# Optimization experiments

Measured on AMD Instinct MI355X. Metric: run time of the kernel, lower is better.

Reference implementation:

```python
import jax, jax.numpy as jnp
import numpy as np

B, G = 128, 20000
HID = 64
NUM_BINS = 10
LEAKY_SLOPE = 0.01  # torch nn.LeakyReLU default


def setup_inputs() -> dict:
    key = jax.random.key(0)
    k1, k2, k3, k4, k5, k6 = jax.random.split(key, 6)
    vals = jax.random.normal(k1, (B, G), dtype=jnp.float32)
    keep = jax.random.uniform(k2, (B, G)) < 0.1
    expr_value = jnp.where(keep, vals, 0.0)
    # MLP params: Linear(1 -> HID), Linear(HID -> NUM_BINS-1)
    W1 = jax.random.normal(k3, (1, HID), dtype=jnp.float32) * 0.5
    b1 = jax.random.normal(k4, (HID,), dtype=jnp.float32) * 0.1
    W2 = jax.random.normal(k5, (HID, NUM_BINS - 1), dtype=jnp.float32) * (1.0 / np.sqrt(HID))
    b2 = jax.random.normal(k6, (NUM_BINS - 1,), dtype=jnp.float32) * 0.1
    return {"expr_value": expr_value, "W1": W1, "b1": b1, "W2": W2, "b2": b2}


def reference(expr_value, W1, b1, W2, b2):
    # mask of nonzero expression positions (B, G)
    mask_expr = (expr_value != 0).astype(jnp.float32)
    # tiny MLP applied to every position (vectorized; zero positions masked out below)
    x = expr_value[..., None]                      # (B, G, 1)
    h = x * W1[0] + b1                             # (B, G, HID); Linear(1->HID)
    h = jnp.where(h >= 0, h, LEAKY_SLOPE * h)      # LeakyReLU
    logits = jnp.einsum('bgh,hk->bgk', h, W2) + b2 # (B, G, NUM_BINS-1)
    p = jax.nn.softmax(logits, axis=-1)            # softmax over bins 1..num_bins-1
    m = mask_expr[..., None]
    # bin 0 prob = 1 where expr==0 else 0; bins 1.. = softmax where expr!=0 else 0
    probs = jnp.concatenate([1.0 - m, p * m], axis=-1)  # (B, G, NUM_BINS)
    return probs, mask_expr
```

## Files before the change

kernel.cpp:

```cpp
#include <hip/hip_runtime.h>
#include <math.h>

#define HID 64
#define KB 9
#define NB 10
#define NTOT (128 * 20000)
#define EPT 2
#define BLOCK 256
#define LEAKY 0.01f
#define RSTRIDE 20
#define TAB_FLOATS (128 + 65 * RSTRIDE)
#define WS_BYTES (TAB_FLOATS * 4)
#define SENT 3.0e38f

typedef float v4f __attribute__((ext_vector_type(4)));

__global__ __launch_bounds__(64) void setup_kernel(
    const float* __restrict__ W1, const float* __restrict__ b1,
    const float* __restrict__ W2, const float* __restrict__ b2,
    float* __restrict__ ws)
{
    __shared__ float t_lds[HID], w_lds[HID], b_lds[HID], tsrt[HID];
    __shared__ float w2_lds[HID * KB];
    __shared__ float red[18 * 65];

    const int j = threadIdx.x;
    const int r = blockIdx.x;
    const float w = W1[j], b = b1[j];
    const float t = (w != 0.0f) ? (-b / w) : -SENT;
    t_lds[j] = t; w_lds[j] = w; b_lds[j] = b;
    #pragma unroll
    for (int q = j; q < HID * KB; q += 64) w2_lds[q] = W2[q];
    __syncthreads();

    int rank = 0;
    for (int i = 0; i < HID; ++i) {
        float ti = t_lds[i];
        rank += (ti < t || (ti == t && i < j)) ? 1 : 0;
    }
    tsrt[rank] = t;
    __syncthreads();

    float xm;
    if (r == 0)        xm = tsrt[0] - 1.0f;
    else if (r == HID) xm = tsrt[HID - 1] + 1.0f;
    else               xm = 0.5f * (tsrt[r - 1] + tsrt[r]);

    const float s = (fmaf(w, xm, b) >= 0.0f) ? 1.0f : LEAKY;
    #pragma unroll
    for (int k = 0; k < KB; ++k) {
        const float w2s = w2_lds[j * KB + k] * s;
        red[(2 * k) * 65 + j]     = w2s * w;
        red[(2 * k + 1) * 65 + j] = w2s * b;
    }
    __syncthreads();

    if (j < 18) {
        float acc = 0.0f;
        for (int i = 0; i < HID; ++i) acc += red[j * 65 + i];
        const int k = j >> 1;
        if (j & 1) ws[128 + r * RSTRIDE + KB + k] = acc + b2[k];
        else       ws[128 + r * RSTRIDE + k]      = acc;
    }
    if (r == 0) { ws[j] = tsrt[j]; ws[64 + j] = SENT; }
}

__global__ __launch_bounds__(BLOCK) void main_kernel(
    const float* __restrict__ expr, const float* __restrict__ ws,
    float* __restrict__ out)
{
    __shared__ float ts[128];
    __shared__ float tab[65 * RSTRIDE];
    __shared__ v4f so[BLOCK * 5];

    const int tid = threadIdx.x;
    for (int t = tid; t < TAB_FLOATS; t += BLOCK) {
        float v = ws[t];
        if (t < 128) ts[t] = v; else tab[t - 128] = v;
    }
    __syncthreads();

    const int i0 = (blockIdx.x * BLOCK + tid) * EPT;
    const float2 xv = *(const float2*)(expr + i0);
    float x[EPT] = {xv.x, xv.y};
    float o[EPT * NB];
    float msk[EPT];
    #pragma unroll
    for (int e = 0; e < EPT; ++e) {
        const float xe = x[e];
        int idx = 0;
        #pragma unroll
        for (int s = 64; s >= 1; s >>= 1)
            idx += (ts[idx + s - 1] <= xe) ? s : 0;
        const v4f* rowv = (const v4f*)(tab + idx * RSTRIDE);
        v4f r0 = rowv[0], r1 = rowv[1], r2 = rowv[2], r3 = rowv[3], r4 = rowv[4];
        const float A[KB] = {r0.x, r0.y, r0.z, r0.w, r1.x, r1.y, r1.z, r1.w, r2.x};
        const float C[KB] = {r2.y, r2.z, r2.w, r3.x, r3.y, r3.z, r3.w, r4.x, r4.y};
        float lg[KB];
        #pragma unroll
        for (int k = 0; k < KB; ++k) lg[k] = fmaf(A[k], xe, C[k]);
        float m = lg[0];
        #pragma unroll
        for (int k = 1; k < KB; ++k) m = fmaxf(m, lg[k]);
        float p[KB];
        float s = 0.0f;
        #pragma unroll
        for (int k = 0; k < KB; ++k) { p[k] = __expf(lg[k] - m); s += p[k]; }
        const float rcp = __frcp_rn(s);
        const bool nz = (xe != 0.0f);
        msk[e] = nz ? 1.0f : 0.0f;
        o[e * NB] = nz ? 0.0f : 1.0f;
        #pragma unroll
        for (int k = 0; k < KB; ++k) o[e * NB + 1 + k] = nz ? p[k] * rcp : 0.0f;
    }

    *(float2*)(out + (size_t)NTOT * NB + i0) = make_float2(msk[0], msk[1]);

    #pragma unroll
    for (int q = 0; q < 5; ++q) so[tid * 5 + q] = ((const v4f*)o)[q];
    __syncthreads();
    float* gout = out + (size_t)blockIdx.x * (BLOCK * EPT * NB);
    #pragma unroll
    for (int q = 0; q < 5; ++q) {
        const int g = q * BLOCK + tid;
        ((v4f*)gout)[g] = so[g];
    }
}

__global__ __launch_bounds__(BLOCK) void fused_kernel(
    const float* __restrict__ expr,
    const float* __restrict__ W1, const float* __restrict__ b1,
    const float* __restrict__ W2, const float* __restrict__ b2,
    float* __restrict__ out)
{
    __shared__ float ts[128];
    __shared__ float tab[65 * RSTRIDE];
    __shared__ float st[HID], sw[HID], sb[HID], tsrt[HID];
    const int tid = threadIdx.x;
    if (tid < HID) {
        float w = W1[tid], b = b1[tid];
        st[tid] = (w != 0.0f) ? (-b / w) : -SENT;
        sw[tid] = w; sb[tid] = b;
    }
    __syncthreads();
    if (tid < HID) {
        float t = st[tid];
        int r = 0;
        for (int i = 0; i < HID; ++i) {
            float ti = st[i];
            r += (ti < t || (ti == t && i < tid)) ? 1 : 0;
        }
        tsrt[r] = t;
    }
    __syncthreads();
    if (tid < 128) ts[tid] = (tid < HID) ? tsrt[tid] : SENT;
    for (int item = tid; item < 65 * KB; item += BLOCK) {
        int r = item / KB, k = item - r * KB;
        float xm;
        if (r == 0)        xm = tsrt[0] - 1.0f;
        else if (r == HID) xm = tsrt[HID - 1] + 1.0f;
        else               xm = 0.5f * (tsrt[r - 1] + tsrt[r]);
        float A = 0.0f, C = b2[k];
        for (int j = 0; j < HID; ++j) {
            float w = sw[j], bb = sb[j];
            float s = (fmaf(w, xm, bb) >= 0.0f) ? 1.0f : LEAKY;
            float w2s = W2[j * KB + k] * s;
            A = fmaf(w2s, w, A);
            C = fmaf(w2s, bb, C);
        }
        tab[r * RSTRIDE + k] = A;
        tab[r * RSTRIDE + KB + k] = C;
    }
    __syncthreads();
    const int i0 = (blockIdx.x * BLOCK + tid) * EPT;
    const float2 xv = *(const float2*)(expr + i0);
    float x[EPT] = {xv.x, xv.y};
    float o[EPT * NB]; float msk[EPT];
    #pragma unroll
    for (int e = 0; e < EPT; ++e) {
        const float xe = x[e];
        int idx = 0;
        #pragma unroll
        for (int s = 64; s >= 1; s >>= 1) idx += (ts[idx + s - 1] <= xe) ? s : 0;
        const float* row = tab + idx * RSTRIDE;
        float lg[KB];
        #pragma unroll
        for (int k = 0; k < KB; ++k) lg[k] = fmaf(row[k], xe, row[KB + k]);
        float m = lg[0];
        #pragma unroll
        for (int k = 1; k < KB; ++k) m = fmaxf(m, lg[k]);
        float p[KB]; float s = 0.0f;
        #pragma unroll
        for (int k = 0; k < KB; ++k) { p[k] = __expf(lg[k] - m); s += p[k]; }
        const float rcp = __frcp_rn(s);
        const bool nz = (xe != 0.0f);
        msk[e] = nz ? 1.0f : 0.0f;
        o[e * NB] = nz ? 0.0f : 1.0f;
        #pragma unroll
        for (int k = 0; k < KB; ++k) o[e * NB + 1 + k] = nz ? p[k] * rcp : 0.0f;
    }
    float* dst = out + (size_t)i0 * NB;
    #pragma unroll
    for (int q = 0; q < EPT * NB / 4; ++q) ((float4*)dst)[q] = ((const float4*)o)[q];
    *(float2*)(out + (size_t)NTOT * NB + i0) = make_float2(msk[0], msk[1]);
}

extern "C" void kernel_launch(void* const* d_in, const int* in_sizes, int n_in,
                              void* d_out, int out_size, void* d_ws, size_t ws_size,
                              hipStream_t stream) {
    const float* expr = (const float*)d_in[0];
    const float* W1   = (const float*)d_in[1];
    const float* b1   = (const float*)d_in[2];
    const float* W2   = (const float*)d_in[3];
    const float* b2   = (const float*)d_in[4];
    float* out = (float*)d_out;
    const int nblocks = NTOT / (BLOCK * EPT);

    if (ws_size >= (size_t)WS_BYTES) {
        float* ws = (float*)d_ws;
        setup_kernel<<<65, 64, 0, stream>>>(W1, b1, W2, b2, ws);
        main_kernel<<<nblocks, BLOCK, 0, stream>>>(expr, ws, out);
    } else {
        fused_kernel<<<nblocks, BLOCK, 0, stream>>>(expr, W1, b1, W2, b2, out);
    }
}
```

Before: 141.6 us.

## Replace binary search with bucket lookup table and fold log2e into logits

```diff
diff --git a/kernel.cpp b/kernel.cpp
--- a/kernel.cpp
+++ b/kernel.cpp
@@ -9,9 +9,17 @@
 #define BLOCK 256
 #define LEAKY 0.01f
 #define RSTRIDE 20
-#define TAB_FLOATS (128 + 65 * RSTRIDE)
-#define WS_BYTES (TAB_FLOATS * 4)
 #define SENT 3.0e38f
+#define LOG2E 1.44269504088896f
+
+#define NBUK 2048
+#define BLO (-6.0f)
+#define BW (12.0f / 2048.0f)
+#define BSCALE (2048.0f / 12.0f)
+
+#define TAB_U32 (128 + 65 * RSTRIDE)
+#define WS_U32 (TAB_U32 + NBUK / 4)
+#define WS_BYTES (WS_U32 * 4)
 
 typedef float v4f __attribute__((ext_vector_type(4)));
 
@@ -25,12 +33,14 @@
     __shared__ float red[18 * 65];
 
     const int j = threadIdx.x;
-    const int r = blockIdx.x;
+    const int blk = blockIdx.x;
     const float w = W1[j], b = b1[j];
     const float t = (w != 0.0f) ? (-b / w) : -SENT;
     t_lds[j] = t; w_lds[j] = w; b_lds[j] = b;
-    #pragma unroll
-    for (int q = j; q < HID * KB; q += 64) w2_lds[q] = W2[q];
+    if (blk < 65) {
+        #pragma unroll
+        for (int q = j; q < HID * KB; q += 64) w2_lds[q] = W2[q];
+    }
     __syncthreads();
 
     int rank = 0;
@@ -41,6 +51,16 @@
     tsrt[rank] = t;
     __syncthreads();
 
+    if (blk >= 65) {
+        const int bb = (blk - 65) * 64 + j;
+        const float edge = BLO + ((float)bb - 0.5f) * BW;
+        int cnt = 0;
+        for (int i = 0; i < HID; ++i) cnt += (tsrt[i] <= edge) ? 1 : 0;
+        ((unsigned char*)(ws + TAB_U32))[bb] = (bb == 0) ? 0 : (unsigned char)cnt;
+        return;
+    }
+
+    const int r = blk;
     float xm;
     if (r == 0)        xm = tsrt[0] - 1.0f;
     else if (r == HID) xm = tsrt[HID - 1] + 1.0f;
@@ -59,8 +79,8 @@
         float acc = 0.0f;
         for (int i = 0; i < HID; ++i) acc += red[j * 65 + i];
         const int k = j >> 1;
-        if (j & 1) ws[128 + r * RSTRIDE + KB + k] = acc + b2[k];
-        else       ws[128 + r * RSTRIDE + k]      = acc;
+        if (j & 1) ws[128 + r * RSTRIDE + KB + k] = (acc + b2[k]) * LOG2E;
+        else       ws[128 + r * RSTRIDE + k]      = acc * LOG2E;
     }
     if (r == 0) { ws[j] = tsrt[j]; ws[64 + j] = SENT; }
 }
@@ -69,16 +89,18 @@
     const float* __restrict__ expr, const float* __restrict__ ws,
     float* __restrict__ out)
 {
-    __shared__ float ts[128];
-    __shared__ float tab[65 * RSTRIDE];
+    __shared__ __align__(16) unsigned int sdata[WS_U32];
     __shared__ v4f so[BLOCK * 5];
 
     const int tid = threadIdx.x;
-    for (int t = tid; t < TAB_FLOATS; t += BLOCK) {
-        float v = ws[t];
-        if (t < 128) ts[t] = v; else tab[t - 128] = v;
-    }
-    __syncthreads();
+    #pragma unroll
+    for (int t = tid; t < WS_U32 / 4; t += BLOCK)
+        ((v4f*)sdata)[t] = ((const v4f*)ws)[t];
+    __syncthreads();
+
+    const float* ts  = (const float*)sdata;
+    const float* tab = (const float*)sdata + 128;
+    const unsigned char* buk = (const unsigned char*)(sdata + TAB_U32);
 
     const int i0 = (blockIdx.x * BLOCK + tid) * EPT;
     const float2 xv = *(const float2*)(expr + i0);
@@ -88,10 +110,9 @@
     #pragma unroll
     for (int e = 0; e < EPT; ++e) {
         const float xe = x[e];
-        int idx = 0;
-        #pragma unroll
-        for (int s = 64; s >= 1; s >>= 1)
-            idx += (ts[idx + s - 1] <= xe) ? s : 0;
+        const float fb = fminf(2047.0f, fmaxf(0.0f, (xe - BLO) * BSCALE));
+        int idx = buk[(int)fb];
+        while (ts[idx] <= xe) ++idx;
         const v4f* rowv = (const v4f*)(tab + idx * RSTRIDE);
         v4f r0 = rowv[0], r1 = rowv[1], r2 = rowv[2], r3 = rowv[3], r4 = rowv[4];
         const float A[KB] = {r0.x, r0.y, r0.z, r0.w, r1.x, r1.y, r1.z, r1.w, r2.x};
@@ -105,7 +126,7 @@
         float p[KB];
         float s = 0.0f;
         #pragma unroll
-        for (int k = 0; k < KB; ++k) { p[k] = __expf(lg[k] - m); s += p[k]; }
+        for (int k = 0; k < KB; ++k) { p[k] = exp2f(lg[k] - m); s += p[k]; }
         const float rcp = __frcp_rn(s);
         const bool nz = (xe != 0.0f);
         msk[e] = nz ? 1.0f : 0.0f;
@@ -218,7 +239,7 @@
 
     if (ws_size >= (size_t)WS_BYTES) {
         float* ws = (float*)d_ws;
-        setup_kernel<<<65, 64, 0, stream>>>(W1, b1, W2, b2, ws);
+        setup_kernel<<<65 + NBUK / 64, 64, 0, stream>>>(W1, b1, W2, b2, ws);
         main_kernel<<<nblocks, BLOCK, 0, stream>>>(expr, ws, out);
     } else {
         fused_kernel<<<nblocks, BLOCK, 0, stream>>>(expr, W1, b1, W2, b2, out);
```

Result: no change. 140.8 us (-0.6%).
